# Kernel tuning notes

Hardware: AMD Instinct MI355X
Metric: run time of the kernel (lower is better)

Reference implementation:

```python
import jax, jax.numpy as jnp
import numpy as np

D = 384      # ViT-S feature dim (feat_dim_lookup['s'])
H = 6        # module forces num_heads = 6
L = 12       # ViT-S depth
RATIO = 0.1  # attention_mask_ratio
EPS = 1e-6


def layernorm(x, g, b):
    m = x.mean(-1, keepdims=True)
    v = ((x - m) ** 2).mean(-1, keepdims=True)
    return (x - m) * jax.lax.rsqrt(v + EPS) * g + b


def masked_attn(x, w_qkv, b_qkv, w_o, b_o):
    # Patch._fix_attn_masking: full softmax attention, threshold at ratio*row_max, renormalize.
    B, N, Dm = x.shape
    dh = Dm // H
    qkv = (x @ w_qkv + b_qkv).reshape(B, N, 3, H, dh)
    q = qkv[:, :, 0].transpose(0, 2, 1, 3)  # [B,H,N,dh]
    k = qkv[:, :, 1].transpose(0, 2, 1, 3)
    v = qkv[:, :, 2].transpose(0, 2, 1, 3)
    scores = jnp.einsum('bhqd,bhkd->bhqk', q, k) * (dh ** -0.5)
    attn = jax.nn.softmax(scores, axis=-1)
    thresh = RATIO * attn.max(axis=-1, keepdims=True)
    attn = jnp.where(attn >= thresh, attn, 0.0)
    attn = attn / attn.sum(axis=-1, keepdims=True)  # re-normalize
    out = jnp.einsum('bhqk,bhkd->bhqd', attn, v)
    out = out.transpose(0, 2, 1, 3).reshape(B, N, Dm)
    return out @ w_o + b_o, attn


def block(x, p):
    w_qkv, b_qkv, w_o, b_o, g1, be1, g2, be2, w1, b1, w2, b2 = p
    h, attn = masked_attn(layernorm(x, g1, be1), w_qkv, b_qkv, w_o, b_o)
    x = x + h
    h = layernorm(x, g2, be2) @ w1 + b1
    h = jax.nn.gelu(h, approximate=False) @ w2 + b2
    return x + h, attn


def setup_inputs() -> dict:
    key = jax.random.key(0)
    ks = jax.random.split(key, 8)
    B, N = 2, 962  # 2 transforms; (1+(160-8)//5)**2 + 1 cls = 962 tokens
    s = 0.02
    return {
        'x': jax.random.normal(ks[0], (B, N, D), jnp.float32),
        'w_qkv': jax.random.normal(ks[1], (L, D, 3 * D), jnp.float32) * s,
        'b_qkv': jnp.zeros((L, 3 * D), jnp.float32),
        'w_proj': jax.random.normal(ks[2], (L, D, D), jnp.float32) * s,
        'b_proj': jnp.zeros((L, D), jnp.float32),
        'ln1_g': jnp.ones((L, D), jnp.float32),
        'ln1_b': jnp.zeros((L, D), jnp.float32),
        'ln2_g': jnp.ones((L, D), jnp.float32),
        'ln2_b': jnp.zeros((L, D), jnp.float32),
        'w_fc1': jax.random.normal(ks[3], (L, D, 4 * D), jnp.float32) * s,
        'b_fc1': jnp.zeros((L, 4 * D), jnp.float32),
        'w_fc2': jax.random.normal(ks[4], (L, 4 * D, D), jnp.float32) * s,
        'b_fc2': jnp.zeros((L, D), jnp.float32),
        'lnf_g': jnp.ones((D,), jnp.float32),
        'lnf_b': jnp.zeros((D,), jnp.float32),
    }


def reference(x, w_qkv, b_qkv, w_proj, b_proj, ln1_g, ln1_b, ln2_g, ln2_b,
              w_fc1, b_fc1, w_fc2, b_fc2, lnf_g, lnf_b):
    params = (w_qkv, b_qkv, w_proj, b_proj, ln1_g, ln1_b, ln2_g, ln2_b,
              w_fc1, b_fc1, w_fc2, b_fc2)
    first = jax.tree_util.tree_map(lambda a: a[:-1], params)
    last = jax.tree_util.tree_map(lambda a: a[-1], params)

    def scan_fn(h, p):
        h, _ = block(h, p)
        return h, None

    x, _ = jax.lax.scan(scan_fn, x, first)  # blocks 0..L-2
    x, attn = block(x, last)                # last block, keep masked attention
    feats = layernorm(x, lnf_g, lnf_b)      # [B, N, D]
    return feats, attn
```

## Files before the change

kernel.cpp:

```cpp
#include <hip/hip_runtime.h>
#include <hip/hip_bf16.h>
#include <math.h>

typedef __bf16 bf16_t;
typedef __bf16 bf16x8 __attribute__((ext_vector_type(8)));
typedef float f32x4 __attribute__((ext_vector_type(4)));

#define NEGBIG -3.0e38f

__global__ void __launch_bounds__(256) tr_k(
    const float* __restrict__ W, bf16_t* __restrict__ Wt, int K, int N)
{
    __shared__ float T[32][33];
    const size_t per = (size_t)K * N;
    const float* Wl = W + blockIdx.z * per;
    bf16_t* Wtl = Wt + blockIdx.z * per;
    int n0 = blockIdx.x * 32, k0 = blockIdx.y * 32;
    int tx = threadIdx.x & 31, ty = threadIdx.x >> 5;
#pragma unroll
    for (int i = 0; i < 4; ++i)
        T[ty + 8 * i][tx] = Wl[(size_t)(k0 + ty + 8 * i) * N + n0 + tx];
    __syncthreads();
#pragma unroll
    for (int i = 0; i < 4; ++i)
        Wtl[(size_t)(n0 + ty + 8 * i) * K + k0 + tx] = (bf16_t)T[tx][ty + 8 * i];
}

template <int MODE>
__global__ void __launch_bounds__(256) gemm_k(
    const bf16_t* __restrict__ A, const bf16_t* __restrict__ Bt,
    const float* __restrict__ bias, int M, int N, int K,
    bf16_t* __restrict__ outb,
    bf16_t* __restrict__ qb, bf16_t* __restrict__ kb, bf16_t* __restrict__ vtb)
{
    __shared__ alignas(16) bf16_t As[2][64][72];
    __shared__ alignas(16) bf16_t Bs[2][64][72];

    const int tid  = threadIdx.x;
    const int wave = tid >> 6, lane = tid & 63;
    const int m0 = blockIdx.y * 64, n0 = blockIdx.x * 64;
    const int rb = (wave >> 1) * 32, cb = (wave & 1) * 32;
    const int q4 = lane >> 4, mm = lane & 15;

    const int lrow = tid >> 3;
    const int lcol = (tid & 7) * 8;

    const bf16_t* pA0 = A  + (size_t)(m0 + lrow) * K + lcol;
    const bf16_t* pA1 = pA0 + (size_t)32 * K;
    const bf16_t* pB0 = Bt + (size_t)(n0 + lrow) * K + lcol;
    const bf16_t* pB1 = pB0 + (size_t)32 * K;

    f32x4 acc[2][2] = {};
    bf16x8 va0, va1, vb0, vb1;

    va0 = *(const bf16x8*)(pA0);
    va1 = *(const bf16x8*)(pA1);
    vb0 = *(const bf16x8*)(pB0);
    vb1 = *(const bf16x8*)(pB1);
    *(bf16x8*)(&As[0][lrow][lcol])      = va0;
    *(bf16x8*)(&As[0][lrow + 32][lcol]) = va1;
    *(bf16x8*)(&Bs[0][lrow][lcol])      = vb0;
    *(bf16x8*)(&Bs[0][lrow + 32][lcol]) = vb1;

    int cur = 0;
    for (int k0 = 0; k0 < K; k0 += 64) {
        __syncthreads();
        const bool has_next = (k0 + 64 < K);
        if (has_next) {
            va0 = *(const bf16x8*)(pA0 + k0 + 64);
            va1 = *(const bf16x8*)(pA1 + k0 + 64);
            vb0 = *(const bf16x8*)(pB0 + k0 + 64);
            vb1 = *(const bf16x8*)(pB1 + k0 + 64);
        }
#pragma unroll
        for (int kc = 0; kc < 64; kc += 32) {
            bf16x8 a0 = *(const bf16x8*)(&As[cur][rb + mm][kc + q4 * 8]);
            bf16x8 a1 = *(const bf16x8*)(&As[cur][rb + 16 + mm][kc + q4 * 8]);
            bf16x8 b0 = *(const bf16x8*)(&Bs[cur][cb + mm][kc + q4 * 8]);
            bf16x8 b1 = *(const bf16x8*)(&Bs[cur][cb + 16 + mm][kc + q4 * 8]);
            acc[0][0] = __builtin_amdgcn_mfma_f32_16x16x32_bf16(a0, b0, acc[0][0], 0, 0, 0);
            acc[0][1] = __builtin_amdgcn_mfma_f32_16x16x32_bf16(a0, b1, acc[0][1], 0, 0, 0);
            acc[1][0] = __builtin_amdgcn_mfma_f32_16x16x32_bf16(a1, b0, acc[1][0], 0, 0, 0);
            acc[1][1] = __builtin_amdgcn_mfma_f32_16x16x32_bf16(a1, b1, acc[1][1], 0, 0, 0);
        }
        if (has_next) {
            int nxt = cur ^ 1;
            *(bf16x8*)(&As[nxt][lrow][lcol])      = va0;
            *(bf16x8*)(&As[nxt][lrow + 32][lcol]) = va1;
            *(bf16x8*)(&Bs[nxt][lrow][lcol])      = vb0;
            *(bf16x8*)(&Bs[nxt][lrow + 32][lcol]) = vb1;
            cur = nxt;
        }
    }

#pragma unroll
    for (int i = 0; i < 2; ++i)
#pragma unroll
    for (int j = 0; j < 2; ++j) {
        int gc = n0 + cb + j * 16 + mm;
        float bv = bias[gc];
#pragma unroll
        for (int r = 0; r < 4; ++r) {
            int gr = m0 + rb + i * 16 + q4 * 4 + r;
            if (gr >= M) continue;
            float val = acc[i][j][r] + bv;
            if (MODE == 2) {
                float g = 0.5f * val * (1.0f + erff(val * 0.70710678118654752f));
                outb[(size_t)gr * N + gc] = (bf16_t)g;
            } else {
                int which = gc / 384, rem = gc % 384;
                int h = rem >> 6, d = rem & 63;
                int b = gr / 962, n = gr % 962;
                int bh = b * 6 + h;
                bf16_t bvv = (bf16_t)val;
                if (which == 0)      qb[((size_t)bh * 962 + n) * 64 + d] = bvv;
                else if (which == 1) kb[((size_t)bh * 962 + n) * 64 + d] = bvv;
                else                 vtb[((size_t)bh * 64 + d) * 992 + n] = bvv;
            }
        }
    }
}

template <int KLEN>
__global__ void __launch_bounds__(256) gemm_sp(
    const bf16_t* __restrict__ A, int lda,
    const bf16_t* __restrict__ Bt, int ldb,
    const float* __restrict__ bias, int M, int N,
    float* __restrict__ resid)
{
    __shared__ alignas(16) bf16_t As[2][64][72];
    __shared__ alignas(16) bf16_t Bs[2][64][72];

    const int tid  = threadIdx.x;
    const int wave = tid >> 6, lane = tid & 63;
    const int m0 = blockIdx.y * 64, n0 = blockIdx.x * 64;
    const int rb = (wave >> 1) * 32, cb = (wave & 1) * 32;
    const int q4 = lane >> 4, mm = lane & 15;
    const int ks = blockIdx.z * KLEN;

    const int lrow = tid >> 3;
    const int lcol = (tid & 7) * 8;

    const bf16_t* pA0 = A  + (size_t)(m0 + lrow) * lda + ks + lcol;
    const bf16_t* pA1 = pA0 + (size_t)32 * lda;
    const bf16_t* pB0 = Bt + (size_t)(n0 + lrow) * ldb + ks + lcol;
    const bf16_t* pB1 = pB0 + (size_t)32 * ldb;

    f32x4 acc[2][2] = {};
    bf16x8 va0, va1, vb0, vb1;

    va0 = *(const bf16x8*)(pA0);
    va1 = *(const bf16x8*)(pA1);
    vb0 = *(const bf16x8*)(pB0);
    vb1 = *(const bf16x8*)(pB1);
    *(bf16x8*)(&As[0][lrow][lcol])      = va0;
    *(bf16x8*)(&As[0][lrow + 32][lcol]) = va1;
    *(bf16x8*)(&Bs[0][lrow][lcol])      = vb0;
    *(bf16x8*)(&Bs[0][lrow + 32][lcol]) = vb1;

    int cur = 0;
    for (int k0 = 0; k0 < KLEN; k0 += 64) {
        __syncthreads();
        const bool has_next = (k0 + 64 < KLEN);
        if (has_next) {
            va0 = *(const bf16x8*)(pA0 + k0 + 64);
            va1 = *(const bf16x8*)(pA1 + k0 + 64);
            vb0 = *(const bf16x8*)(pB0 + k0 + 64);
            vb1 = *(const bf16x8*)(pB1 + k0 + 64);
        }
#pragma unroll
        for (int kc = 0; kc < 64; kc += 32) {
            bf16x8 a0 = *(const bf16x8*)(&As[cur][rb + mm][kc + q4 * 8]);
            bf16x8 a1 = *(const bf16x8*)(&As[cur][rb + 16 + mm][kc + q4 * 8]);
            bf16x8 b0 = *(const bf16x8*)(&Bs[cur][cb + mm][kc + q4 * 8]);
            bf16x8 b1 = *(const bf16x8*)(&Bs[cur][cb + 16 + mm][kc + q4 * 8]);
            acc[0][0] = __builtin_amdgcn_mfma_f32_16x16x32_bf16(a0, b0, acc[0][0], 0, 0, 0);
            acc[0][1] = __builtin_amdgcn_mfma_f32_16x16x32_bf16(a0, b1, acc[0][1], 0, 0, 0);
            acc[1][0] = __builtin_amdgcn_mfma_f32_16x16x32_bf16(a1, b0, acc[1][0], 0, 0, 0);
            acc[1][1] = __builtin_amdgcn_mfma_f32_16x16x32_bf16(a1, b1, acc[1][1], 0, 0, 0);
        }
        if (has_next) {
            int nxt = cur ^ 1;
            *(bf16x8*)(&As[nxt][lrow][lcol])      = va0;
            *(bf16x8*)(&As[nxt][lrow + 32][lcol]) = va1;
            *(bf16x8*)(&Bs[nxt][lrow][lcol])      = vb0;
            *(bf16x8*)(&Bs[nxt][lrow + 32][lcol]) = vb1;
            cur = nxt;
        }
    }

#pragma unroll
    for (int i = 0; i < 2; ++i)
#pragma unroll
    for (int j = 0; j < 2; ++j) {
        int gc = n0 + cb + j * 16 + mm;
        float bv = (blockIdx.z == 0) ? bias[gc] : 0.f;
#pragma unroll
        for (int r = 0; r < 4; ++r) {
            int gr = m0 + rb + i * 16 + q4 * 4 + r;
            if (gr >= M) continue;
            atomicAdd(&resid[(size_t)gr * N + gc], acc[i][j][r] + bv);
        }
    }
}

__global__ void __launch_bounds__(256) attn_k(
    const bf16_t* __restrict__ qb, const bf16_t* __restrict__ kb,
    const bf16_t* __restrict__ vtb, bf16_t* __restrict__ attnout,
    float* __restrict__ attn_save)
{
    __shared__ alignas(16) bf16_t S[16][1000];

    const int tid  = threadIdx.x;
    const int wave = tid >> 6, lane = tid & 63;
    const int q4 = lane >> 4, mm = lane & 15;
    const int bh = blockIdx.y, qt = blockIdx.x;
    const int qrow0 = qt * 16;

    int qr = qrow0 + mm; if (qr > 961) qr = 961;
    const bf16_t* qptr = qb + ((size_t)bh * 962 + qr) * 64 + q4 * 8;
    bf16x8 aq0 = *(const bf16x8*)(qptr);
    bf16x8 aq1 = *(const bf16x8*)(qptr + 32);

    for (int ct = wave; ct < 61; ct += 4) {
        int kr = ct * 16 + mm; if (kr > 961) kr = 961;
        const bf16_t* kptr = kb + ((size_t)bh * 962 + kr) * 64 + q4 * 8;
        bf16x8 b0 = *(const bf16x8*)(kptr);
        bf16x8 b1 = *(const bf16x8*)(kptr + 32);
        f32x4 acc = {};
        acc = __builtin_amdgcn_mfma_f32_16x16x32_bf16(aq0, b0, acc, 0, 0, 0);
        acc = __builtin_amdgcn_mfma_f32_16x16x32_bf16(aq1, b1, acc, 0, 0, 0);
        int col = ct * 16 + mm;
#pragma unroll
        for (int r = 0; r < 4; ++r) {
            int row = q4 * 4 + r;
            if (col < 962) S[row][col] = (bf16_t)(acc[r] * 0.125f);
        }
    }
    for (int idx = tid; idx < 16 * 38; idx += 256) {
        int r = idx / 38, c = 962 + idx % 38;
        S[r][c] = (bf16_t)NEGBIG;
    }
    __syncthreads();

    const int trow = tid >> 4, ti = tid & 15;
    float e[8][8];
    float mx = NEGBIG;
#pragma unroll
    for (int t = 0; t < 8; ++t) {
        int c8 = ti * 8 + 128 * t;
        bf16x8 xv;
        if (c8 < 1000) xv = *(const bf16x8*)(&S[trow][c8]);
        else {
#pragma unroll
            for (int j = 0; j < 8; ++j) xv[j] = (bf16_t)NEGBIG;
        }
#pragma unroll
        for (int j = 0; j < 8; ++j) { e[t][j] = (float)xv[j]; mx = fmaxf(mx, e[t][j]); }
    }
#pragma unroll
    for (int off = 8; off > 0; off >>= 1) mx = fmaxf(mx, __shfl_xor(mx, off, 16));

    float sum = 0.f;
#pragma unroll
    for (int t = 0; t < 8; ++t)
#pragma unroll
    for (int j = 0; j < 8; ++j) {
        float ev = __expf(e[t][j] - mx);
        e[t][j] = ev;
        if (ev >= 0.1f) sum += ev;
    }
#pragma unroll
    for (int off = 8; off > 0; off >>= 1) sum += __shfl_xor(sum, off, 16);
    float inv = 1.0f / sum;

    int row_g = qrow0 + trow;
#pragma unroll
    for (int t = 0; t < 8; ++t) {
        int c8 = ti * 8 + 128 * t;
        if (c8 >= 1000) continue;
        bf16x8 pv;
#pragma unroll
        for (int j = 0; j < 8; ++j) {
            float pp = (e[t][j] >= 0.1f) ? e[t][j] * inv : 0.f;
            e[t][j] = pp;
            pv[j] = (bf16_t)pp;
        }
        *(bf16x8*)(&S[trow][c8]) = pv;
        if (attn_save && row_g < 962) {
#pragma unroll
            for (int j = 0; j < 8; ++j)
                if (c8 + j < 962)
                    attn_save[((size_t)bh * 962 + row_g) * 962 + c8 + j] = e[t][j];
        }
    }
    __syncthreads();

    const int wc0 = wave * 16;
    f32x4 o = {};
    for (int kc = 0; kc < 31; ++kc) {
        bf16x8 pa = *(const bf16x8*)(&S[mm][kc * 32 + q4 * 8]);
        bf16x8 vb = *(const bf16x8*)(vtb + ((size_t)bh * 64 + wc0 + mm) * 992 + kc * 32 + q4 * 8);
        o = __builtin_amdgcn_mfma_f32_16x16x32_bf16(pa, vb, o, 0, 0, 0);
    }
    int b = bh / 6, h = bh % 6;
#pragma unroll
    for (int r = 0; r < 4; ++r) {
        int qrr = qrow0 + q4 * 4 + r;
        if (qrr < 962)
            attnout[((size_t)(b * 962 + qrr)) * 384 + h * 64 + wc0 + mm] = (bf16_t)o[r];
    }
}

template <typename OT>
__global__ void __launch_bounds__(256) ln_k(
    const float* __restrict__ x, const float* __restrict__ g,
    const float* __restrict__ b, OT* __restrict__ out)
{
    int t = blockIdx.x * 4 + (threadIdx.x >> 6);
    int lane = threadIdx.x & 63;
    const float* xp = x + (size_t)t * 384;
    float v[6];
    float s = 0.f;
#pragma unroll
    for (int i = 0; i < 6; ++i) { v[i] = xp[lane + 64 * i]; s += v[i]; }
    for (int off = 32; off > 0; off >>= 1) s += __shfl_xor(s, off);
    float mean = s * (1.0f / 384.0f);
    float s2 = 0.f;
#pragma unroll
    for (int i = 0; i < 6; ++i) { float d = v[i] - mean; s2 += d * d; }
    for (int off = 32; off > 0; off >>= 1) s2 += __shfl_xor(s2, off);
    float rstd = rsqrtf(s2 * (1.0f / 384.0f) + 1e-6f);
#pragma unroll
    for (int i = 0; i < 6; ++i) {
        int c = lane + 64 * i;
        float y = (v[i] - mean) * rstd * g[c] + b[c];
        out[(size_t)t * 384 + c] = (OT)y;
    }
}

extern "C" void kernel_launch(void* const* d_in, const int* in_sizes, int n_in,
                              void* d_out, int out_size, void* d_ws, size_t ws_size,
                              hipStream_t stream)
{
    const float* xin    = (const float*)d_in[0];
    const float* w_qkv  = (const float*)d_in[1];
    const float* b_qkv  = (const float*)d_in[2];
    const float* w_proj = (const float*)d_in[3];
    const float* b_proj = (const float*)d_in[4];
    const float* ln1g   = (const float*)d_in[5];
    const float* ln1b   = (const float*)d_in[6];
    const float* ln2g   = (const float*)d_in[7];
    const float* ln2b   = (const float*)d_in[8];
    const float* w_fc1  = (const float*)d_in[9];
    const float* b_fc1  = (const float*)d_in[10];
    const float* w_fc2  = (const float*)d_in[11];
    const float* b_fc2  = (const float*)d_in[12];
    const float* lnfg   = (const float*)d_in[13];
    const float* lnfb   = (const float*)d_in[14];

    float* feats     = (float*)d_out;
    float* attn_save = feats + 738816;

    char* p = (char*)d_ws;
    auto alloc = [&](size_t bytes) {
        char* r = p;
        p += (bytes + 255) & ~(size_t)255;
        return r;
    };
    float*  x_f32   = (float*)alloc(1924ull * 384 * 4);
    bf16_t* xn      = (bf16_t*)alloc(1984ull * 384 * 2);
    bf16_t* qbuf    = (bf16_t*)alloc(12ull * 962 * 64 * 2);
    bf16_t* kbuf    = (bf16_t*)alloc(12ull * 962 * 64 * 2);
    bf16_t* vtbuf   = (bf16_t*)alloc(12ull * 64 * 992 * 2);
    bf16_t* attnout = (bf16_t*)alloc(1984ull * 384 * 2);
    bf16_t* mlp1    = (bf16_t*)alloc(1984ull * 1536 * 2);
    bf16_t* wt_qkv  = (bf16_t*)alloc(12ull * 1152 * 384 * 2);
    bf16_t* wt_proj = (bf16_t*)alloc(12ull * 384 * 384 * 2);
    bf16_t* wt_fc1  = (bf16_t*)alloc(12ull * 1536 * 384 * 2);
    bf16_t* wt_fc2  = (bf16_t*)alloc(12ull * 384 * 1536 * 2);

    tr_k<<<dim3(36, 12, 12), dim3(256), 0, stream>>>(w_qkv,  wt_qkv,  384, 1152);
    tr_k<<<dim3(12, 12, 12), dim3(256), 0, stream>>>(w_proj, wt_proj, 384, 384);
    tr_k<<<dim3(48, 12, 12), dim3(256), 0, stream>>>(w_fc1,  wt_fc1,  384, 1536);
    tr_k<<<dim3(12, 48, 12), dim3(256), 0, stream>>>(w_fc2,  wt_fc2,  1536, 384);

    hipMemcpyAsync(x_f32, xin, 738816ull * 4, hipMemcpyDeviceToDevice, stream);

    for (int l = 0; l < 12; ++l) {
        ln_k<bf16_t><<<dim3(481), dim3(256), 0, stream>>>(x_f32, ln1g + l * 384, ln1b + l * 384, xn);
        gemm_k<0><<<dim3(18, 31), dim3(256), 0, stream>>>(
            xn, wt_qkv + (size_t)l * 1152 * 384, b_qkv + l * 1152,
            1924, 1152, 384, nullptr, qbuf, kbuf, vtbuf);
        attn_k<<<dim3(61, 12), dim3(256), 0, stream>>>(
            qbuf, kbuf, vtbuf, attnout, (l == 11) ? attn_save : (float*)nullptr);
        gemm_sp<192><<<dim3(6, 31, 2), dim3(256), 0, stream>>>(
            attnout, 384, wt_proj + (size_t)l * 384 * 384, 384, b_proj + l * 384,
            1924, 384, x_f32);
        ln_k<bf16_t><<<dim3(481), dim3(256), 0, stream>>>(x_f32, ln2g + l * 384, ln2b + l * 384, xn);
        gemm_k<2><<<dim3(24, 31), dim3(256), 0, stream>>>(
            xn, wt_fc1 + (size_t)l * 1536 * 384, b_fc1 + l * 1536,
            1924, 1536, 384, mlp1, nullptr, nullptr, nullptr);
        gemm_sp<384><<<dim3(6, 31, 4), dim3(256), 0, stream>>>(
            mlp1, 1536, wt_fc2 + (size_t)l * 384 * 1536, 1536, b_fc2 + l * 384,
            1924, 384, x_f32);
    }
    ln_k<float><<<dim3(481), dim3(256), 0, stream>>>(x_f32, lnfg, lnfb, feats);
}
```

Baseline: 1.062 ms.

## Fuse LayerNorm into QKV and FC1 GEMM prologue with full-K A tile

Removes the separate LayerNorm kernels before the QKV and FC1 GEMMs. Each GEMM block now reads its 64 fp32 rows, computes the row statistics, and writes the normalized bf16 rows as a full-K A tile in shared memory, then streams only B tiles. This saves two launches per layer and the bf16 round trip of the normalized activations. In exchange, each row's LayerNorm is recomputed by every column block (18 or 24 times), and the larger shared-memory footprint may reduce occupancy.

Measured after the change: 1.192 ms. +12.2%, slower.

```diff
diff --git a/kernel.cpp b/kernel.cpp
--- a/kernel.cpp
+++ b/kernel.cpp
@@ -4,6 +4,7 @@
 
 typedef __bf16 bf16_t;
 typedef __bf16 bf16x8 __attribute__((ext_vector_type(8)));
+typedef __bf16 bf16x4 __attribute__((ext_vector_type(4)));
 typedef float f32x4 __attribute__((ext_vector_type(4)));
 
 #define NEGBIG -3.0e38f
@@ -27,13 +28,15 @@
 }
 
 template <int MODE>
-__global__ void __launch_bounds__(256) gemm_k(
-    const bf16_t* __restrict__ A, const bf16_t* __restrict__ Bt,
-    const float* __restrict__ bias, int M, int N, int K,
+__global__ void __launch_bounds__(256) gemm_ln(
+    const float* __restrict__ X, const float* __restrict__ G,
+    const float* __restrict__ Bb,
+    const bf16_t* __restrict__ Bt, const float* __restrict__ bias,
+    int M, int N,
     bf16_t* __restrict__ outb,
     bf16_t* __restrict__ qb, bf16_t* __restrict__ kb, bf16_t* __restrict__ vtb)
 {
-    __shared__ alignas(16) bf16_t As[2][64][72];
+    __shared__ alignas(16) bf16_t As[64][392];
     __shared__ alignas(16) bf16_t Bs[2][64][72];
 
     const int tid  = threadIdx.x;
@@ -42,40 +45,69 @@
     const int rb = (wave >> 1) * 32, cb = (wave & 1) * 32;
     const int q4 = lane >> 4, mm = lane & 15;
 
+    {
+        const int rr  = tid >> 3;
+        const int sub = tid & 7;
+#pragma unroll
+        for (int c = 0; c < 2; ++c) {
+            int r = c * 32 + rr;
+            int grow = m0 + r; if (grow > 1923) grow = 1923;
+            const float* xp = X + (size_t)grow * 384;
+            f32x4 v[12];
+            float s = 0.f;
+#pragma unroll
+            for (int i = 0; i < 12; ++i) {
+                v[i] = *(const f32x4*)(xp + ((sub + 8 * i) << 2));
+                s += v[i][0] + v[i][1] + v[i][2] + v[i][3];
+            }
+            s += __shfl_xor(s, 1); s += __shfl_xor(s, 2); s += __shfl_xor(s, 4);
+            float mean = s * (1.0f / 384.0f);
+            float s2 = 0.f;
+#pragma unroll
+            for (int i = 0; i < 12; ++i) {
+#pragma unroll
+                for (int j = 0; j < 4; ++j) { float d = v[i][j] - mean; s2 += d * d; }
+            }
+            s2 += __shfl_xor(s2, 1); s2 += __shfl_xor(s2, 2); s2 += __shfl_xor(s2, 4);
+            float rstd = rsqrtf(s2 * (1.0f / 384.0f) + 1e-6f);
+#pragma unroll
+            for (int i = 0; i < 12; ++i) {
+                int col = (sub + 8 * i) << 2;
+                f32x4 g4 = *(const f32x4*)(G + col);
+                f32x4 b4 = *(const f32x4*)(Bb + col);
+                bf16x4 o;
+#pragma unroll
+                for (int j = 0; j < 4; ++j)
+                    o[j] = (bf16_t)((v[i][j] - mean) * rstd * g4[j] + b4[j]);
+                *(bf16x4*)(&As[r][col]) = o;
+            }
+        }
+    }
+
     const int lrow = tid >> 3;
     const int lcol = (tid & 7) * 8;
 
-    const bf16_t* pA0 = A  + (size_t)(m0 + lrow) * K + lcol;
-    const bf16_t* pA1 = pA0 + (size_t)32 * K;
-    const bf16_t* pB0 = Bt + (size_t)(n0 + lrow) * K + lcol;
-    const bf16_t* pB1 = pB0 + (size_t)32 * K;
+    const bf16_t* pB0 = Bt + (size_t)(n0 + lrow) * 384 + lcol;
+    const bf16_t* pB1 = pB0 + (size_t)32 * 384;
 
     f32x4 acc[2][2] = {};
-    bf16x8 va0, va1, vb0, vb1;
-
-    va0 = *(const bf16x8*)(pA0);
-    va1 = *(const bf16x8*)(pA1);
-    vb0 = *(const bf16x8*)(pB0);
-    vb1 = *(const bf16x8*)(pB1);
-    *(bf16x8*)(&As[0][lrow][lcol])      = va0;
-    *(bf16x8*)(&As[0][lrow + 32][lcol]) = va1;
+    bf16x8 vb0 = *(const bf16x8*)(pB0);
+    bf16x8 vb1 = *(const bf16x8*)(pB1);
     *(bf16x8*)(&Bs[0][lrow][lcol])      = vb0;
     *(bf16x8*)(&Bs[0][lrow + 32][lcol]) = vb1;
 
     int cur = 0;
-    for (int k0 = 0; k0 < K; k0 += 64) {
+    for (int k0 = 0; k0 < 384; k0 += 64) {
         __syncthreads();
-        const bool has_next = (k0 + 64 < K);
+        const bool has_next = (k0 + 64 < 384);
         if (has_next) {
-            va0 = *(const bf16x8*)(pA0 + k0 + 64);
-            va1 = *(const bf16x8*)(pA1 + k0 + 64);
             vb0 = *(const bf16x8*)(pB0 + k0 + 64);
             vb1 = *(const bf16x8*)(pB1 + k0 + 64);
         }
 #pragma unroll
         for (int kc = 0; kc < 64; kc += 32) {
-            bf16x8 a0 = *(const bf16x8*)(&As[cur][rb + mm][kc + q4 * 8]);
-            bf16x8 a1 = *(const bf16x8*)(&As[cur][rb + 16 + mm][kc + q4 * 8]);
+            bf16x8 a0 = *(const bf16x8*)(&As[rb + mm][k0 + kc + q4 * 8]);
+            bf16x8 a1 = *(const bf16x8*)(&As[rb + 16 + mm][k0 + kc + q4 * 8]);
             bf16x8 b0 = *(const bf16x8*)(&Bs[cur][cb + mm][kc + q4 * 8]);
             bf16x8 b1 = *(const bf16x8*)(&Bs[cur][cb + 16 + mm][kc + q4 * 8]);
             acc[0][0] = __builtin_amdgcn_mfma_f32_16x16x32_bf16(a0, b0, acc[0][0], 0, 0, 0);
@@ -85,8 +117,6 @@
         }
         if (has_next) {
             int nxt = cur ^ 1;
-            *(bf16x8*)(&As[nxt][lrow][lcol])      = va0;
-            *(bf16x8*)(&As[nxt][lrow + 32][lcol]) = va1;
             *(bf16x8*)(&Bs[nxt][lrow][lcol])      = vb0;
             *(bf16x8*)(&Bs[nxt][lrow + 32][lcol]) = vb1;
             cur = nxt;
@@ -369,7 +399,6 @@
         return r;
     };
     float*  x_f32   = (float*)alloc(1924ull * 384 * 4);
-    bf16_t* xn      = (bf16_t*)alloc(1984ull * 384 * 2);
     bf16_t* qbuf    = (bf16_t*)alloc(12ull * 962 * 64 * 2);
     bf16_t* kbuf    = (bf16_t*)alloc(12ull * 962 * 64 * 2);
     bf16_t* vtbuf   = (bf16_t*)alloc(12ull * 64 * 992 * 2);
@@ -388,19 +417,19 @@
     hipMemcpyAsync(x_f32, xin, 738816ull * 4, hipMemcpyDeviceToDevice, stream);
 
     for (int l = 0; l < 12; ++l) {
-        ln_k<bf16_t><<<dim3(481), dim3(256), 0, stream>>>(x_f32, ln1g + l * 384, ln1b + l * 384, xn);
-        gemm_k<0><<<dim3(18, 31), dim3(256), 0, stream>>>(
-            xn, wt_qkv + (size_t)l * 1152 * 384, b_qkv + l * 1152,
-            1924, 1152, 384, nullptr, qbuf, kbuf, vtbuf);
+        gemm_ln<0><<<dim3(18, 31), dim3(256), 0, stream>>>(
+            x_f32, ln1g + l * 384, ln1b + l * 384,
+            wt_qkv + (size_t)l * 1152 * 384, b_qkv + l * 1152,
+            1924, 1152, nullptr, qbuf, kbuf, vtbuf);
         attn_k<<<dim3(61, 12), dim3(256), 0, stream>>>(
             qbuf, kbuf, vtbuf, attnout, (l == 11) ? attn_save : (float*)nullptr);
         gemm_sp<192><<<dim3(6, 31, 2), dim3(256), 0, stream>>>(
             attnout, 384, wt_proj + (size_t)l * 384 * 384, 384, b_proj + l * 384,
             1924, 384, x_f32);
-        ln_k<bf16_t><<<dim3(481), dim3(256), 0, stream>>>(x_f32, ln2g + l * 384, ln2b + l * 384, xn);
-        gemm_k<2><<<dim3(24, 31), dim3(256), 0, stream>>>(
-            xn, wt_fc1 + (size_t)l * 1536 * 384, b_fc1 + l * 1536,
-            1924, 1536, 384, mlp1, nullptr, nullptr, nullptr);
+        gemm_ln<2><<<dim3(24, 31), dim3(256), 0, stream>>>(
+            x_f32, ln2g + l * 384, ln2b + l * 384,
+            wt_fc1 + (size_t)l * 1536 * 384, b_fc1 + l * 1536,
+            1924, 1536, mlp1, nullptr, nullptr, nullptr);
         gemm_sp<384><<<dim3(6, 31, 4), dim3(256), 0, stream>>>(
             mlp1, 1536, wt_fc2 + (size_t)l * 384 * 1536, 1536, b_fc2 + l * 384,
             1924, 384, x_f32);
```
